# Performance work log

Hardware: AMD Instinct MI355X
Metric: run time of the kernel (lower is better)

Reference implementation:

```python
import jax, jax.numpy as jnp
import numpy as np

GAMMA = 0.99
GAE_LAMBDA = 0.95
CLIP_PARAM = 0.2
VALUE_LOSS_COEF = 0.5
ENTROPY_COEF = 0.01
T, N = 1024, 8192

def setup_inputs() -> dict:
    key = jax.random.key(0)
    ks = jax.random.split(key, 9)
    rewards = jax.random.normal(ks[0], (T, N, 1), dtype=jnp.float32)
    masks = (jax.random.uniform(ks[1], (T + 1, N, 1)) > 0.02).astype(jnp.float32)
    bad_masks = (jax.random.uniform(ks[2], (T + 1, N, 1)) > 0.01).astype(jnp.float32)
    value_preds = jax.random.normal(ks[3], (T + 1, N, 1), dtype=jnp.float32)
    last_value = jax.random.normal(ks[4], (N, 1), dtype=jnp.float32)
    log_prob = jax.random.normal(ks[5], (T, N, 1), dtype=jnp.float32) * 0.1
    prev_log_prob = jax.random.normal(ks[6], (T, N, 1), dtype=jnp.float32) * 0.1
    new_value = jax.random.normal(ks[7], (T, N, 1), dtype=jnp.float32)
    dist_entropy = jax.random.normal(ks[8], (T, N, 1), dtype=jnp.float32)
    return {"rewards": rewards, "masks": masks, "bad_masks": bad_masks,
            "value_preds": value_preds, "last_value": last_value,
            "log_prob": log_prob, "prev_log_prob": prev_log_prob,
            "new_value": new_value, "dist_entropy": dist_entropy}


def _compute_derived(rewards, masks, bad_masks, value_preds, last_value):
    # value_preds is detached in the original update(); mirror with stop_gradient
    vp = jax.lax.stop_gradient(value_preds)
    lv = jax.lax.stop_gradient(last_value)
    vp = vp.at[-1].set(lv)  # value_preds[-1] = last_value

    def step(gae, xs):
        r, v_next, v, m_next, bad_next = xs
        delta = r + GAMMA * v_next * m_next - v
        gae = (delta + GAMMA * GAE_LAMBDA * m_next * gae) * bad_next
        return gae, gae + v  # returns[step] = gae + value_preds[step]

    xs = (rewards, vp[1:], vp[:-1], masks[1:], bad_masks[1:])
    init = jnp.zeros_like(lv)
    _, returns_t = jax.lax.scan(step, init, xs, reverse=True)  # (T, N, 1)

    advantages = returns_t - vp[:-1]
    advantages = (advantages - advantages.mean()) / (advantages.std(ddof=1) + 1e-5)
    return advantages, returns_t


def reference(rewards, masks, bad_masks, value_preds, last_value,
              log_prob, prev_log_prob, new_value, dist_entropy):
    advantages, returns_t = _compute_derived(rewards, masks, bad_masks,
                                             value_preds, last_value)
    # PPO clipped surrogate (single minibatch = full rollout, flattened over T*N)
    ratio = jnp.exp(log_prob - prev_log_prob)
    surr1 = ratio * advantages
    surr2 = jnp.clip(ratio, 1.0 - CLIP_PARAM, 1.0 + CLIP_PARAM) * advantages
    action_loss = -jnp.minimum(surr1, surr2).mean()

    value_target = jax.lax.stop_gradient(returns_t)
    old_value = jax.lax.stop_gradient(value_preds[:-1])
    value_pred_clipped = old_value + jnp.clip(new_value - old_value,
                                              -CLIP_PARAM, CLIP_PARAM)
    value_losses = (new_value - value_target) ** 2
    value_losses_clipped = (value_pred_clipped - value_target) ** 2
    value_loss = 0.5 * jnp.maximum(value_losses, value_losses_clipped).mean()

    loss = (value_loss * VALUE_LOSS_COEF + action_loss
            - dist_entropy.mean() * ENTROPY_COEF)
    return loss
```

## Files before the change

### kernel.cpp

```cpp
#include <hip/hip_runtime.h>
#include <math.h>

#define T_DIM 1024
#define N_DIM 8192
#define M_TOT (T_DIM * N_DIM)
#define NV4   (N_DIM / 4)
#define L_CHUNK 4
#define C_CHUNKS (T_DIM / L_CHUNK)
#define PC_BLOCKS ((C_CHUNKS * NV4) / 256)
#define SCAN_BLOCKS ((NV4 * 32) / 256)

#define kGAMMA 0.99f
#define kGLAM  (0.99f * 0.95f)


__device__ __forceinline__ unsigned short f2bf(float f) {
    unsigned int u = __float_as_uint(f);
    u += 0x7fffu + ((u >> 16) & 1u);
    return (unsigned short)(u >> 16);
}
__device__ __forceinline__ float bf2f(unsigned short h) {
    return __uint_as_float(((unsigned int)h) << 16);
}

__global__ __launch_bounds__(256, 6) void k_pc(
    const float4* __restrict__ r4,
    const float4* __restrict__ m4,
    const float4* __restrict__ bm4,
    const float4* __restrict__ vp4,
    const float4* __restrict__ lv4,
    ushort4* __restrict__ b16,
    float4* __restrict__ A_out,
    float4* __restrict__ B_out)
{
    const int g  = blockIdx.x * 256 + threadIdx.x;
    const int j  = g & (NV4 - 1);
    const int c  = g >> 11;
    const int t0 = c * L_CHUNK;
    const bool last_c = (c == C_CHUNKS - 1);

    float4 Aa = make_float4(1.f, 1.f, 1.f, 1.f);
    float4 Bb = make_float4(0.f, 0.f, 0.f, 0.f);

    #pragma unroll
    for (int i = L_CHUNK - 1; i >= 0; --i) {
        const int idx = (t0 + i) * NV4 + j;
        const float4 r  = r4[idx];
        const float4 v  = vp4[idx];
        const float4 vn = (last_c && i == L_CHUNK - 1) ? lv4[j]
                                                       : vp4[idx + NV4];
        const float4 m  = m4[idx + NV4];
        const float4 bb = bm4[idx + NV4];

        ushort4 o;
        {
            const float b = (fmaf(kGAMMA * m.x, vn.x, r.x) - v.x) * bb.x;
            const float a = kGLAM * m.x * bb.x;
            Aa.x = a * Aa.x; Bb.x = fmaf(a, Bb.x, b);
            o.x = (unsigned short)((f2bf(b) & 0xFFFEu) | ((m.x * bb.x > 0.5f) ? 1u : 0u));
        }
        {
            const float b = (fmaf(kGAMMA * m.y, vn.y, r.y) - v.y) * bb.y;
            const float a = kGLAM * m.y * bb.y;
            Aa.y = a * Aa.y; Bb.y = fmaf(a, Bb.y, b);
            o.y = (unsigned short)((f2bf(b) & 0xFFFEu) | ((m.y * bb.y > 0.5f) ? 1u : 0u));
        }
        {
            const float b = (fmaf(kGAMMA * m.z, vn.z, r.z) - v.z) * bb.z;
            const float a = kGLAM * m.z * bb.z;
            Aa.z = a * Aa.z; Bb.z = fmaf(a, Bb.z, b);
            o.z = (unsigned short)((f2bf(b) & 0xFFFEu) | ((m.z * bb.z > 0.5f) ? 1u : 0u));
        }
        {
            const float b = (fmaf(kGAMMA * m.w, vn.w, r.w) - v.w) * bb.w;
            const float a = kGLAM * m.w * bb.w;
            Aa.w = a * Aa.w; Bb.w = fmaf(a, Bb.w, b);
            o.w = (unsigned short)((f2bf(b) & 0xFFFEu) | ((m.w * bb.w > 0.5f) ? 1u : 0u));
        }
        b16[idx] = o;
    }
    A_out[c * NV4 + j] = Aa;
    B_out[c * NV4 + j] = Bb;
}

__global__ __launch_bounds__(256, 4) void k_scan(
    float4* __restrict__ Ag,
    const float4* __restrict__ Bg)
{
    const int u  = blockIdx.x * 256 + threadIdx.x;
    const int jj = u >> 5;
    const int k  = u & 31;

    float4 As[8], Bs[8];
    #pragma unroll
    for (int i = 0; i < 8; ++i) {
        As[i] = Ag[(8 * k + i) * NV4 + jj];
        Bs[i] = Bg[(8 * k + i) * NV4 + jj];
    }
    float4 Pa = As[7], Pb = Bs[7];
    #pragma unroll
    for (int i = 6; i >= 0; --i) {
        Pb.x = fmaf(As[i].x, Pb.x, Bs[i].x); Pa.x = As[i].x * Pa.x;
        Pb.y = fmaf(As[i].y, Pb.y, Bs[i].y); Pa.y = As[i].y * Pa.y;
        Pb.z = fmaf(As[i].z, Pb.z, Bs[i].z); Pa.z = As[i].z * Pa.z;
        Pb.w = fmaf(As[i].w, Pb.w, Bs[i].w); Pa.w = As[i].w * Pa.w;
    }
    #pragma unroll
    for (int d = 1; d < 32; d <<= 1) {
        const float nax = __shfl_down(Pa.x, d, 32), nay = __shfl_down(Pa.y, d, 32);
        const float naz = __shfl_down(Pa.z, d, 32), naw = __shfl_down(Pa.w, d, 32);
        const float nbx = __shfl_down(Pb.x, d, 32), nby = __shfl_down(Pb.y, d, 32);
        const float nbz = __shfl_down(Pb.z, d, 32), nbw = __shfl_down(Pb.w, d, 32);
        if (k + d < 32) {
            Pb.x = fmaf(Pa.x, nbx, Pb.x); Pa.x *= nax;
            Pb.y = fmaf(Pa.y, nby, Pb.y); Pa.y *= nay;
            Pb.z = fmaf(Pa.z, nbz, Pb.z); Pa.z *= naz;
            Pb.w = fmaf(Pa.w, nbw, Pb.w); Pa.w *= naw;
        }
    }
    float4 G;
    G.x = __shfl_down(Pb.x, 1, 32);
    G.y = __shfl_down(Pb.y, 1, 32);
    G.z = __shfl_down(Pb.z, 1, 32);
    G.w = __shfl_down(Pb.w, 1, 32);
    if (k == 31) G = make_float4(0.f, 0.f, 0.f, 0.f);
    #pragma unroll
    for (int i = 7; i >= 0; --i) {
        Ag[(8 * k + i) * NV4 + jj] = G;
        G.x = fmaf(As[i].x, G.x, Bs[i].x);
        G.y = fmaf(As[i].y, G.y, Bs[i].y);
        G.z = fmaf(As[i].z, G.z, Bs[i].z);
        G.w = fmaf(As[i].w, G.w, Bs[i].w);
    }
}

__device__ __forceinline__ void gae_comp(float& gae, unsigned short h,
                                         float v, float nvv,
                                         float& sg, float& sg2, float& v_s) {
    const float bf = bf2f(h);
    const float a  = (h & 1u) ? kGLAM : 0.0f;
    gae = fmaf(a, gae, bf);
    sg += gae;
    sg2 = fmaf(gae, gae, sg2);
    const float q  = nvv - v;
    const float e1 = q - gae;
    const float e2 = fminf(fmaxf(q, -0.2f), 0.2f) - gae;
    v_s += fmaxf(e1 * e1, e2 * e2);
}

__global__ __launch_bounds__(256, 8) void k_gae(
    const ushort4* __restrict__ b16,
    const float4* __restrict__ g_in4,
    const float4* __restrict__ vp4,
    const float4* __restrict__ nv4,
    double* __restrict__ pg)
{
    const int g  = blockIdx.x * 256 + threadIdx.x;
    const int j  = g & (NV4 - 1);
    const int c  = g >> 11;
    const int t0 = c * L_CHUNK;

    float4 gae = g_in4[c * NV4 + j];
    float sg = 0.f, sg2 = 0.f, v_s = 0.f;

    #pragma unroll
    for (int i = L_CHUNK - 1; i >= 0; --i) {
        const int idx = (t0 + i) * NV4 + j;
        const ushort4 h = b16[idx];
        const float4  v = vp4[idx];
        const float4  q = nv4[idx];
        gae_comp(gae.x, h.x, v.x, q.x, sg, sg2, v_s);
        gae_comp(gae.y, h.y, v.y, q.y, sg, sg2, v_s);
        gae_comp(gae.z, h.z, v.z, q.z, sg, sg2, v_s);
        gae_comp(gae.w, h.w, v.w, q.w, sg, sg2, v_s);
    }

    double d0 = (double)sg, d1 = (double)sg2, d2 = (double)v_s;
    #pragma unroll
    for (int off = 32; off > 0; off >>= 1) {
        d0 += __shfl_down(d0, off, 64);
        d1 += __shfl_down(d1, off, 64);
        d2 += __shfl_down(d2, off, 64);
    }
    __shared__ double sh[3][4];
    const int wid = threadIdx.x >> 6, lane = threadIdx.x & 63;
    if (lane == 0) { sh[0][wid] = d0; sh[1][wid] = d1; sh[2][wid] = d2; }
    __syncthreads();
    if (threadIdx.x == 0) {
        double t0s = 0, t1s = 0, t2s = 0;
        #pragma unroll
        for (int w = 0; w < 4; ++w) { t0s += sh[0][w]; t1s += sh[1][w]; t2s += sh[2][w]; }
        pg[blockIdx.x * 3 + 0] = t0s;
        pg[blockIdx.x * 3 + 1] = t1s;
        pg[blockIdx.x * 3 + 2] = t2s;
    }
}

__global__ __launch_bounds__(256, 6) void k_loss(
    const ushort4* __restrict__ b16,
    const float4* __restrict__ g_in4,
    const float4* __restrict__ lp4,
    const float4* __restrict__ plp4,
    const float4* __restrict__ ent4,
    const double* __restrict__ pg,
    double* __restrict__ pl)
{
    __shared__ double sh[2][4];
    __shared__ double bc[2];
    const int tid = threadIdx.x;

    {
        double s0 = 0.0, s1 = 0.0;
        for (int i = tid; i < PC_BLOCKS; i += 256) {
            s0 += pg[i * 3 + 0];
            s1 += pg[i * 3 + 1];
        }
        #pragma unroll
        for (int off = 32; off > 0; off >>= 1) {
            s0 += __shfl_down(s0, off, 64);
            s1 += __shfl_down(s1, off, 64);
        }
        const int wid = tid >> 6, lane = tid & 63;
        if (lane == 0) { sh[0][wid] = s0; sh[1][wid] = s1; }
        __syncthreads();
        if (tid == 0) {
            double sum = 0, sum2 = 0;
            #pragma unroll
            for (int w = 0; w < 4; ++w) { sum += sh[0][w]; sum2 += sh[1][w]; }
            const double M = (double)M_TOT;
            const double mu = sum / M;
            double var = (sum2 - sum * sum / M) / (M - 1.0);
            if (var < 0.0) var = 0.0;
            bc[0] = mu;
            bc[1] = 1.0 / (sqrt(var) + 1e-5);
        }
        __syncthreads();
    }
    const float mu   = (float)bc[0];
    const float invs = (float)bc[1];

    const int g  = blockIdx.x * 256 + tid;
    const int j  = g & (NV4 - 1);
    const int c  = g >> 11;
    const int t0 = c * L_CHUNK;

    float4 gv = g_in4[c * NV4 + j];
    float a_s = 0.f, e_s = 0.f;

    #pragma unroll
    for (int i = L_CHUNK - 1; i >= 0; --i) {
        const int idx = (t0 + i) * NV4 + j;
        const ushort4 h = b16[idx];
        const float4 Lp = lp4[idx];
        const float4 Pp = plp4[idx];
        const float4 E  = ent4[idx];
#define P5C(comp, H) { \
        const unsigned short hh = (H); \
        const float bf = bf2f(hh); \
        const float a  = (hh & 1u) ? kGLAM : 0.0f; \
        gv.comp = fmaf(a, gv.comp, bf); \
        const float x  = (gv.comp - mu) * invs; \
        const float rr = __expf(Lp.comp - Pp.comp); \
        const float rc = fminf(fmaxf(rr, 0.8f), 1.2f); \
        a_s += fminf(rr * x, rc * x); }
        P5C(x, h.x) P5C(y, h.y) P5C(z, h.z) P5C(w, h.w)
#undef P5C
        e_s += E.x + E.y + E.z + E.w;
    }

    double d0 = (double)a_s, d1 = (double)e_s;
    #pragma unroll
    for (int off = 32; off > 0; off >>= 1) {
        d0 += __shfl_down(d0, off, 64);
        d1 += __shfl_down(d1, off, 64);
    }
    const int wid = tid >> 6, lane = tid & 63;
    if (lane == 0) { sh[0][wid] = d0; sh[1][wid] = d1; }
    __syncthreads();
    if (tid == 0) {
        double t0s = 0, t1s = 0;
        #pragma unroll
        for (int w = 0; w < 4; ++w) { t0s += sh[0][w]; t1s += sh[1][w]; }
        pl[blockIdx.x * 2 + 0] = t0s;
        pl[blockIdx.x * 2 + 1] = t1s;
    }
}

__global__ __launch_bounds__(256) void k_final(
    const double* __restrict__ pg, const double* __restrict__ pl,
    float* __restrict__ out)
{
    double s0 = 0.0, s1 = 0.0, s2 = 0.0;
    for (int i = threadIdx.x; i < PC_BLOCKS; i += 256) {
        s0 += pl[i * 2 + 0];
        s1 += pl[i * 2 + 1];
        s2 += pg[i * 3 + 2];
    }
    #pragma unroll
    for (int off = 32; off > 0; off >>= 1) {
        s0 += __shfl_down(s0, off, 64);
        s1 += __shfl_down(s1, off, 64);
        s2 += __shfl_down(s2, off, 64);
    }
    __shared__ double sh[3][4];
    const int wid = threadIdx.x >> 6, lane = threadIdx.x & 63;
    if (lane == 0) { sh[0][wid] = s0; sh[1][wid] = s1; sh[2][wid] = s2; }
    __syncthreads();
    if (threadIdx.x == 0) {
        double a_sum = 0, e_sum = 0, vsum = 0;
        #pragma unroll
        for (int w = 0; w < 4; ++w) { a_sum += sh[0][w]; e_sum += sh[1][w]; vsum += sh[2][w]; }
        const double M = (double)M_TOT;
        out[0] = (float)(0.25 * vsum / M - a_sum / M - 0.01 * e_sum / M);
    }
}

extern "C" void kernel_launch(void* const* d_in, const int* in_sizes, int n_in,
                              void* d_out, int out_size, void* d_ws, size_t ws_size,
                              hipStream_t stream) {
    const float* rewards     = (const float*)d_in[0];
    const float* masks       = (const float*)d_in[1];
    const float* bad_masks   = (const float*)d_in[2];
    const float* value_preds = (const float*)d_in[3];
    const float* last_value  = (const float*)d_in[4];
    const float* log_prob    = (const float*)d_in[5];
    const float* prev_lp     = (const float*)d_in[6];
    const float* new_value   = (const float*)d_in[7];
    const float* dist_ent    = (const float*)d_in[8];

    char* ws = (char*)d_ws;
    double* pg = (double*)(ws + 1024);
    double* pl = (double*)(ws + 65536);
    unsigned short* b16 = (unsigned short*)(ws + 131072);
    float* A = (float*)(ws + 131072 + (size_t)M_TOT * 2);
    float* B = (float*)(ws + 131072 + (size_t)M_TOT * 2 + (size_t)C_CHUNKS * N_DIM * 4);

    k_pc<<<PC_BLOCKS, 256, 0, stream>>>((const float4*)rewards,
                                        (const float4*)masks,
                                        (const float4*)bad_masks,
                                        (const float4*)value_preds,
                                        (const float4*)last_value,
                                        (ushort4*)b16, (float4*)A, (float4*)B);
    k_scan<<<SCAN_BLOCKS, 256, 0, stream>>>((float4*)A, (const float4*)B);
    k_gae<<<PC_BLOCKS, 256, 0, stream>>>((const ushort4*)b16,
                                         (const float4*)A ,
                                         (const float4*)value_preds,
                                         (const float4*)new_value, pg);
    k_loss<<<PC_BLOCKS, 256, 0, stream>>>((const ushort4*)b16,
                                          (const float4*)A ,
                                          (const float4*)log_prob,
                                          (const float4*)prev_lp,
                                          (const float4*)dist_ent, pg, pl);
    k_final<<<1, 256, 0, stream>>>(pg, pl, (float*)d_out);
}
```

Baseline: 274.0 us.

## Double chunk length, batch loads, reuse next value, hoist stats into separate kernel

Raises the per-thread time chunk from 4 to 8 steps, which halves the number of chunk carries written by the first pass and scanned by the second, and shrinks the per-thread work in the scan kernel. The first pass now carries the next value-pred in a register instead of reloading it, and loads are batched ahead of the arithmetic to raise memory-level parallelism. The mean/std reduction that every k_loss block used to redo from all partials is moved into a single-block k_stats kernel, at the cost of one extra launch. Larger chunks mean fewer threads and more registers per thread, so occupancy bounds were retuned.

Result: no change. 272.5 us (-0.6%).

```diff
diff --git a/kernel.cpp b/kernel.cpp
--- a/kernel.cpp
+++ b/kernel.cpp
@@ -5,7 +5,7 @@
 #define N_DIM 8192
 #define M_TOT (T_DIM * N_DIM)
 #define NV4   (N_DIM / 4)
-#define L_CHUNK 4
+#define L_CHUNK 8
 #define C_CHUNKS (T_DIM / L_CHUNK)
 #define PC_BLOCKS ((C_CHUNKS * NV4) / 256)
 #define SCAN_BLOCKS ((NV4 * 32) / 256)
@@ -23,7 +23,7 @@
     return __uint_as_float(((unsigned int)h) << 16);
 }
 
-__global__ __launch_bounds__(256, 6) void k_pc(
+__global__ __launch_bounds__(256, 4) void k_pc(
     const float4* __restrict__ r4,
     const float4* __restrict__ m4,
     const float4* __restrict__ bm4,
@@ -37,53 +37,42 @@
     const int j  = g & (NV4 - 1);
     const int c  = g >> 11;
     const int t0 = c * L_CHUNK;
-    const bool last_c = (c == C_CHUNKS - 1);
-
+
+    float4 vnext = (c == C_CHUNKS - 1) ? lv4[j] : vp4[(t0 + L_CHUNK) * NV4 + j];
     float4 Aa = make_float4(1.f, 1.f, 1.f, 1.f);
     float4 Bb = make_float4(0.f, 0.f, 0.f, 0.f);
 
     #pragma unroll
-    for (int i = L_CHUNK - 1; i >= 0; --i) {
-        const int idx = (t0 + i) * NV4 + j;
-        const float4 r  = r4[idx];
-        const float4 v  = vp4[idx];
-        const float4 vn = (last_c && i == L_CHUNK - 1) ? lv4[j]
-                                                       : vp4[idx + NV4];
-        const float4 m  = m4[idx + NV4];
-        const float4 bb = bm4[idx + NV4];
-
-        ushort4 o;
-        {
-            const float b = (fmaf(kGAMMA * m.x, vn.x, r.x) - v.x) * bb.x;
-            const float a = kGLAM * m.x * bb.x;
-            Aa.x = a * Aa.x; Bb.x = fmaf(a, Bb.x, b);
-            o.x = (unsigned short)((f2bf(b) & 0xFFFEu) | ((m.x * bb.x > 0.5f) ? 1u : 0u));
-        }
-        {
-            const float b = (fmaf(kGAMMA * m.y, vn.y, r.y) - v.y) * bb.y;
-            const float a = kGLAM * m.y * bb.y;
-            Aa.y = a * Aa.y; Bb.y = fmaf(a, Bb.y, b);
-            o.y = (unsigned short)((f2bf(b) & 0xFFFEu) | ((m.y * bb.y > 0.5f) ? 1u : 0u));
-        }
-        {
-            const float b = (fmaf(kGAMMA * m.z, vn.z, r.z) - v.z) * bb.z;
-            const float a = kGLAM * m.z * bb.z;
-            Aa.z = a * Aa.z; Bb.z = fmaf(a, Bb.z, b);
-            o.z = (unsigned short)((f2bf(b) & 0xFFFEu) | ((m.z * bb.z > 0.5f) ? 1u : 0u));
-        }
-        {
-            const float b = (fmaf(kGAMMA * m.w, vn.w, r.w) - v.w) * bb.w;
-            const float a = kGLAM * m.w * bb.w;
-            Aa.w = a * Aa.w; Bb.w = fmaf(a, Bb.w, b);
-            o.w = (unsigned short)((f2bf(b) & 0xFFFEu) | ((m.w * bb.w > 0.5f) ? 1u : 0u));
-        }
-        b16[idx] = o;
+    for (int half = 0; half < 2; ++half) {
+        const int ibase = (half == 0) ? 7 : 3;
+        float4 R[4], V[4], M[4], BBv[4];
+        #pragma unroll
+        for (int u = 0; u < 4; ++u) {
+            const int idx = (t0 + ibase - u) * NV4 + j;
+            R[u]   = r4[idx];
+            V[u]   = vp4[idx];
+            M[u]   = m4[idx + NV4];
+            BBv[u] = bm4[idx + NV4];
+        }
+        #pragma unroll
+        for (int u = 0; u < 4; ++u) {
+            ushort4 o;
+#define P1C(comp) { \
+            const float b = (fmaf(kGAMMA * M[u].comp, vnext.comp, R[u].comp) - V[u].comp) * BBv[u].comp; \
+            const float a = kGLAM * M[u].comp * BBv[u].comp; \
+            Aa.comp = a * Aa.comp; Bb.comp = fmaf(a, Bb.comp, b); \
+            o.comp = (unsigned short)((f2bf(b) & 0xFFFEu) | ((M[u].comp * BBv[u].comp > 0.5f) ? 1u : 0u)); }
+            P1C(x) P1C(y) P1C(z) P1C(w)
+#undef P1C
+            b16[(t0 + ibase - u) * NV4 + j] = o;
+            vnext = V[u];
+        }
     }
     A_out[c * NV4 + j] = Aa;
     B_out[c * NV4 + j] = Bb;
 }
 
-__global__ __launch_bounds__(256, 4) void k_scan(
+__global__ __launch_bounds__(256, 8) void k_scan(
     float4* __restrict__ Ag,
     const float4* __restrict__ Bg)
 {
@@ -91,15 +80,15 @@
     const int jj = u >> 5;
     const int k  = u & 31;
 
-    float4 As[8], Bs[8];
-    #pragma unroll
-    for (int i = 0; i < 8; ++i) {
-        As[i] = Ag[(8 * k + i) * NV4 + jj];
-        Bs[i] = Bg[(8 * k + i) * NV4 + jj];
-    }
-    float4 Pa = As[7], Pb = Bs[7];
-    #pragma unroll
-    for (int i = 6; i >= 0; --i) {
+    float4 As[4], Bs[4];
+    #pragma unroll
+    for (int i = 0; i < 4; ++i) {
+        As[i] = Ag[(4 * k + i) * NV4 + jj];
+        Bs[i] = Bg[(4 * k + i) * NV4 + jj];
+    }
+    float4 Pa = As[3], Pb = Bs[3];
+    #pragma unroll
+    for (int i = 2; i >= 0; --i) {
         Pb.x = fmaf(As[i].x, Pb.x, Bs[i].x); Pa.x = As[i].x * Pa.x;
         Pb.y = fmaf(As[i].y, Pb.y, Bs[i].y); Pa.y = As[i].y * Pa.y;
         Pb.z = fmaf(As[i].z, Pb.z, Bs[i].z); Pa.z = As[i].z * Pa.z;
@@ -125,8 +114,8 @@
     G.w = __shfl_down(Pb.w, 1, 32);
     if (k == 31) G = make_float4(0.f, 0.f, 0.f, 0.f);
     #pragma unroll
-    for (int i = 7; i >= 0; --i) {
-        Ag[(8 * k + i) * NV4 + jj] = G;
+    for (int i = 3; i >= 0; --i) {
+        Ag[(4 * k + i) * NV4 + jj] = G;
         G.x = fmaf(As[i].x, G.x, Bs[i].x);
         G.y = fmaf(As[i].y, G.y, Bs[i].y);
         G.z = fmaf(As[i].z, G.z, Bs[i].z);
@@ -134,21 +123,7 @@
     }
 }
 
-__device__ __forceinline__ void gae_comp(float& gae, unsigned short h,
-                                         float v, float nvv,
-                                         float& sg, float& sg2, float& v_s) {
-    const float bf = bf2f(h);
-    const float a  = (h & 1u) ? kGLAM : 0.0f;
-    gae = fmaf(a, gae, bf);
-    sg += gae;
-    sg2 = fmaf(gae, gae, sg2);
-    const float q  = nvv - v;
-    const float e1 = q - gae;
-    const float e2 = fminf(fmaxf(q, -0.2f), 0.2f) - gae;
-    v_s += fmaxf(e1 * e1, e2 * e2);
-}
-
-__global__ __launch_bounds__(256, 8) void k_gae(
+__global__ __launch_bounds__(256, 4) void k_gae(
     const ushort4* __restrict__ b16,
     const float4* __restrict__ g_in4,
     const float4* __restrict__ vp4,
@@ -163,16 +138,28 @@
     float4 gae = g_in4[c * NV4 + j];
     float sg = 0.f, sg2 = 0.f, v_s = 0.f;
 
-    #pragma unroll
-    for (int i = L_CHUNK - 1; i >= 0; --i) {
-        const int idx = (t0 + i) * NV4 + j;
-        const ushort4 h = b16[idx];
-        const float4  v = vp4[idx];
-        const float4  q = nv4[idx];
-        gae_comp(gae.x, h.x, v.x, q.x, sg, sg2, v_s);
-        gae_comp(gae.y, h.y, v.y, q.y, sg, sg2, v_s);
-        gae_comp(gae.z, h.z, v.z, q.z, sg, sg2, v_s);
-        gae_comp(gae.w, h.w, v.w, q.w, sg, sg2, v_s);
+    ushort4 H[8]; float4 V[8], Q[8];
+    #pragma unroll
+    for (int u = 0; u < 8; ++u) {
+        const int idx = (t0 + 7 - u) * NV4 + j;
+        H[u] = b16[idx];
+        V[u] = vp4[idx];
+        Q[u] = nv4[idx];
+    }
+    #pragma unroll
+    for (int u = 0; u < 8; ++u) {
+#define P3C(comp, HH) { \
+        const unsigned short h = (HH); \
+        const float bf = bf2f(h); \
+        const float a  = (h & 1u) ? kGLAM : 0.0f; \
+        gae.comp = fmaf(a, gae.comp, bf); \
+        sg += gae.comp; sg2 = fmaf(gae.comp, gae.comp, sg2); \
+        const float qd = Q[u].comp - V[u].comp; \
+        const float e1 = qd - gae.comp; \
+        const float e2 = fminf(fmaxf(qd, -0.2f), 0.2f) - gae.comp; \
+        v_s += fmaxf(e1 * e1, e2 * e2); }
+        P3C(x, H[u].x) P3C(y, H[u].y) P3C(z, H[u].z) P3C(w, H[u].w)
+#undef P3C
     }
 
     double d0 = (double)sg, d1 = (double)sg2, d2 = (double)v_s;
@@ -196,76 +183,87 @@
     }
 }
 
-__global__ __launch_bounds__(256, 6) void k_loss(
+__global__ __launch_bounds__(256) void k_stats(
+    const double* __restrict__ pg, double* __restrict__ acc)
+{
+    double s0 = 0.0, s1 = 0.0, s2 = 0.0;
+    for (int i = threadIdx.x; i < PC_BLOCKS; i += 256) {
+        s0 += pg[i * 3 + 0];
+        s1 += pg[i * 3 + 1];
+        s2 += pg[i * 3 + 2];
+    }
+    #pragma unroll
+    for (int off = 32; off > 0; off >>= 1) {
+        s0 += __shfl_down(s0, off, 64);
+        s1 += __shfl_down(s1, off, 64);
+        s2 += __shfl_down(s2, off, 64);
+    }
+    __shared__ double sh[3][4];
+    const int wid = threadIdx.x >> 6, lane = threadIdx.x & 63;
+    if (lane == 0) { sh[0][wid] = s0; sh[1][wid] = s1; sh[2][wid] = s2; }
+    __syncthreads();
+    if (threadIdx.x == 0) {
+        double sum = 0, sum2 = 0, vsum = 0;
+        #pragma unroll
+        for (int w = 0; w < 4; ++w) { sum += sh[0][w]; sum2 += sh[1][w]; vsum += sh[2][w]; }
+        const double M = (double)M_TOT;
+        const double mu = sum / M;
+        double var = (sum2 - sum * sum / M) / (M - 1.0);
+        if (var < 0.0) var = 0.0;
+        acc[3] = vsum;
+        acc[5] = mu;
+        acc[6] = 1.0 / (sqrt(var) + 1e-5);
+    }
+}
+
+__global__ __launch_bounds__(256, 4) void k_loss(
     const ushort4* __restrict__ b16,
     const float4* __restrict__ g_in4,
     const float4* __restrict__ lp4,
     const float4* __restrict__ plp4,
     const float4* __restrict__ ent4,
-    const double* __restrict__ pg,
+    const double* __restrict__ acc,
     double* __restrict__ pl)
 {
-    __shared__ double sh[2][4];
-    __shared__ double bc[2];
     const int tid = threadIdx.x;
-
-    {
-        double s0 = 0.0, s1 = 0.0;
-        for (int i = tid; i < PC_BLOCKS; i += 256) {
-            s0 += pg[i * 3 + 0];
-            s1 += pg[i * 3 + 1];
-        }
-        #pragma unroll
-        for (int off = 32; off > 0; off >>= 1) {
-            s0 += __shfl_down(s0, off, 64);
-            s1 += __shfl_down(s1, off, 64);
-        }
-        const int wid = tid >> 6, lane = tid & 63;
-        if (lane == 0) { sh[0][wid] = s0; sh[1][wid] = s1; }
-        __syncthreads();
-        if (tid == 0) {
-            double sum = 0, sum2 = 0;
-            #pragma unroll
-            for (int w = 0; w < 4; ++w) { sum += sh[0][w]; sum2 += sh[1][w]; }
-            const double M = (double)M_TOT;
-            const double mu = sum / M;
-            double var = (sum2 - sum * sum / M) / (M - 1.0);
-            if (var < 0.0) var = 0.0;
-            bc[0] = mu;
-            bc[1] = 1.0 / (sqrt(var) + 1e-5);
-        }
-        __syncthreads();
-    }
-    const float mu   = (float)bc[0];
-    const float invs = (float)bc[1];
-
     const int g  = blockIdx.x * 256 + tid;
     const int j  = g & (NV4 - 1);
     const int c  = g >> 11;
     const int t0 = c * L_CHUNK;
 
+    const float mu   = (float)acc[5];
+    const float invs = (float)acc[6];
+
     float4 gv = g_in4[c * NV4 + j];
     float a_s = 0.f, e_s = 0.f;
 
     #pragma unroll
-    for (int i = L_CHUNK - 1; i >= 0; --i) {
-        const int idx = (t0 + i) * NV4 + j;
-        const ushort4 h = b16[idx];
-        const float4 Lp = lp4[idx];
-        const float4 Pp = plp4[idx];
-        const float4 E  = ent4[idx];
-#define P5C(comp, H) { \
-        const unsigned short hh = (H); \
-        const float bf = bf2f(hh); \
-        const float a  = (hh & 1u) ? kGLAM : 0.0f; \
-        gv.comp = fmaf(a, gv.comp, bf); \
-        const float x  = (gv.comp - mu) * invs; \
-        const float rr = __expf(Lp.comp - Pp.comp); \
-        const float rc = fminf(fmaxf(rr, 0.8f), 1.2f); \
-        a_s += fminf(rr * x, rc * x); }
-        P5C(x, h.x) P5C(y, h.y) P5C(z, h.z) P5C(w, h.w)
+    for (int half = 0; half < 2; ++half) {
+        const int ibase = (half == 0) ? 7 : 3;
+        ushort4 H[4]; float4 L[4], P[4], E[4];
+        #pragma unroll
+        for (int u = 0; u < 4; ++u) {
+            const int idx = (t0 + ibase - u) * NV4 + j;
+            H[u] = b16[idx];
+            L[u] = lp4[idx];
+            P[u] = plp4[idx];
+            E[u] = ent4[idx];
+        }
+        #pragma unroll
+        for (int u = 0; u < 4; ++u) {
+#define P5C(comp, HH) { \
+            const unsigned short hh = (HH); \
+            const float bf = bf2f(hh); \
+            const float a  = (hh & 1u) ? kGLAM : 0.0f; \
+            gv.comp = fmaf(a, gv.comp, bf); \
+            const float x  = (gv.comp - mu) * invs; \
+            const float rr = __expf(L[u].comp - P[u].comp); \
+            const float rc = fminf(fmaxf(rr, 0.8f), 1.2f); \
+            a_s += fminf(rr * x, rc * x); }
+            P5C(x, H[u].x) P5C(y, H[u].y) P5C(z, H[u].z) P5C(w, H[u].w)
 #undef P5C
-        e_s += E.x + E.y + E.z + E.w;
+            e_s += E[u].x + E[u].y + E[u].z + E[u].w;
+        }
     }
 
     double d0 = (double)a_s, d1 = (double)e_s;
@@ -274,6 +272,7 @@
         d0 += __shfl_down(d0, off, 64);
         d1 += __shfl_down(d1, off, 64);
     }
+    __shared__ double sh[2][4];
     const int wid = tid >> 6, lane = tid & 63;
     if (lane == 0) { sh[0][wid] = d0; sh[1][wid] = d1; }
     __syncthreads();
@@ -287,31 +286,29 @@
 }
 
 __global__ __launch_bounds__(256) void k_final(
-    const double* __restrict__ pg, const double* __restrict__ pl,
+    const double* __restrict__ pl, const double* __restrict__ acc,
     float* __restrict__ out)
 {
-    double s0 = 0.0, s1 = 0.0, s2 = 0.0;
+    double s0 = 0.0, s1 = 0.0;
     for (int i = threadIdx.x; i < PC_BLOCKS; i += 256) {
         s0 += pl[i * 2 + 0];
         s1 += pl[i * 2 + 1];
-        s2 += pg[i * 3 + 2];
     }
     #pragma unroll
     for (int off = 32; off > 0; off >>= 1) {
         s0 += __shfl_down(s0, off, 64);
         s1 += __shfl_down(s1, off, 64);
-        s2 += __shfl_down(s2, off, 64);
-    }
-    __shared__ double sh[3][4];
+    }
+    __shared__ double sh[2][4];
     const int wid = threadIdx.x >> 6, lane = threadIdx.x & 63;
-    if (lane == 0) { sh[0][wid] = s0; sh[1][wid] = s1; sh[2][wid] = s2; }
+    if (lane == 0) { sh[0][wid] = s0; sh[1][wid] = s1; }
     __syncthreads();
     if (threadIdx.x == 0) {
-        double a_sum = 0, e_sum = 0, vsum = 0;
-        #pragma unroll
-        for (int w = 0; w < 4; ++w) { a_sum += sh[0][w]; e_sum += sh[1][w]; vsum += sh[2][w]; }
+        double a_sum = 0, e_sum = 0;
+        #pragma unroll
+        for (int w = 0; w < 4; ++w) { a_sum += sh[0][w]; e_sum += sh[1][w]; }
         const double M = (double)M_TOT;
-        out[0] = (float)(0.25 * vsum / M - a_sum / M - 0.01 * e_sum / M);
+        out[0] = (float)(0.25 * acc[3] / M - a_sum / M - 0.01 * e_sum / M);
     }
 }
 
@@ -329,11 +326,12 @@
     const float* dist_ent    = (const float*)d_in[8];
 
     char* ws = (char*)d_ws;
-    double* pg = (double*)(ws + 1024);
-    double* pl = (double*)(ws + 65536);
-    unsigned short* b16 = (unsigned short*)(ws + 131072);
-    float* A = (float*)(ws + 131072 + (size_t)M_TOT * 2);
-    float* B = (float*)(ws + 131072 + (size_t)M_TOT * 2 + (size_t)C_CHUNKS * N_DIM * 4);
+    double* acc = (double*)ws;
+    double* pg  = (double*)(ws + 256);
+    double* pl  = (double*)(ws + 32768);
+    unsigned short* b16 = (unsigned short*)(ws + 65536);
+    float* A = (float*)(ws + 65536 + (size_t)M_TOT * 2);
+    float* B = (float*)(ws + 65536 + (size_t)M_TOT * 2 + (size_t)C_CHUNKS * N_DIM * 4);
 
     k_pc<<<PC_BLOCKS, 256, 0, stream>>>((const float4*)rewards,
                                         (const float4*)masks,
@@ -346,10 +344,11 @@
                                          (const float4*)A ,
                                          (const float4*)value_preds,
                                          (const float4*)new_value, pg);
+    k_stats<<<1, 256, 0, stream>>>(pg, acc);
     k_loss<<<PC_BLOCKS, 256, 0, stream>>>((const ushort4*)b16,
                                           (const float4*)A ,
                                           (const float4*)log_prob,
                                           (const float4*)prev_lp,
-                                          (const float4*)dist_ent, pg, pl);
-    k_final<<<1, 256, 0, stream>>>(pg, pl, (float*)d_out);
-}
+                                          (const float4*)dist_ent, acc, pl);
+    k_final<<<1, 256, 0, stream>>>(pl, acc, (float*)d_out);
+}
```
